# Kernel tuning notes

Measured on AMD Instinct MI355X. Metric: run time of the kernel, lower is better.

The kernel has to match this reference:

```python
import jax, jax.numpy as jnp
import numpy as np

BN_EPS = 1e-5
N_NODES = 100000
N_EDGES = 1600000
D = 128


def setup_inputs() -> dict:
    key = jax.random.key(0)
    ks = jax.random.split(key, 8)
    h = jax.random.normal(ks[0], (N_NODES, D), dtype=jnp.float32)
    snorm_n = jax.random.uniform(ks[1], (N_NODES, 1), dtype=jnp.float32)
    eps = jnp.zeros((1,), dtype=jnp.float32)
    W1 = jax.random.normal(ks[2], (D, D), dtype=jnp.float32) * (1.0 / np.sqrt(D))
    b1 = jnp.zeros((D,), dtype=jnp.float32)
    W2 = jax.random.normal(ks[3], (D, D), dtype=jnp.float32) * (1.0 / np.sqrt(D))
    b2 = jnp.zeros((D,), dtype=jnp.float32)
    bn_gamma = jnp.ones((D,), dtype=jnp.float32)
    bn_beta = jnp.zeros((D,), dtype=jnp.float32)
    src = jax.random.randint(ks[4], (N_EDGES,), 0, N_NODES, dtype=jnp.int32)
    dst = jax.random.randint(ks[5], (N_EDGES,), 0, N_NODES, dtype=jnp.int32)
    return {"h": h, "snorm_n": snorm_n, "eps": eps, "W1": W1, "b1": b1,
            "W2": W2, "b2": b2, "bn_gamma": bn_gamma, "bn_beta": bn_beta,
            "src": src, "dst": dst}


def reference(h, snorm_n, eps, W1, b1, W2, b2, bn_gamma, bn_beta, src, dst):
    h_in = h
    # message passing: copy_u + sum reduce -> scatter-add of h[src] into dst
    neigh = jax.ops.segment_sum(h[src], dst, num_segments=N_NODES)  # [N, D]
    x = (1.0 + eps[0]) * h + neigh
    # apply_func: 2-layer MLP (Linear -> ReLU -> Linear)
    x = jax.nn.relu(x @ W1 + b1) @ W2 + b2
    # graph norm w.r.t. graph sizes
    x = x * snorm_n
    # batch norm (training-mode batch statistics over nodes)
    mean = jnp.mean(x, axis=0)
    var = jnp.var(x, axis=0)
    x = (x - mean) * jax.lax.rsqrt(var + BN_EPS) * bn_gamma + bn_beta
    x = jax.nn.relu(x)
    # residual (in_dim == out_dim)
    x = h_in + x
    # dropout p=0.0 -> identity
    return x
```

## Files before the change

### kernel.cpp

```cpp
#include <hip/hip_runtime.h>

#define D 128
#define NN 100000
#define NE 1600000
#define SCAN_NBLK 98
#define GT_ROWS 128
#define GEMM_NT ((NN + GT_ROWS - 1) / GT_ROWS)
#define GEMM_GRID 256

__global__ __launch_bounds__(256) void count_kernel(
    const int* __restrict__ dst, int* __restrict__ cnt)
{
    int g4 = blockIdx.x * 256 + threadIdx.x;
    if (g4 >= NE / 4) return;
    int4 d = ((const int4*)dst)[g4];
    atomicAdd(&cnt[d.x], 1);
    atomicAdd(&cnt[d.y], 1);
    atomicAdd(&cnt[d.z], 1);
    atomicAdd(&cnt[d.w], 1);
}

__global__ __launch_bounds__(256) void scan_local_kernel(
    const int* __restrict__ cnt, int* __restrict__ pre, int* __restrict__ blkSum)
{
    __shared__ int lds[256];
    const int t = threadIdx.x;
    const int base = blockIdx.x * 1024 + t * 4;
    int4 v = {0, 0, 0, 0};
    if (base + 3 < NN) v = *(const int4*)&cnt[base];
    else {
        if (base + 0 < NN) v.x = cnt[base + 0];
        if (base + 1 < NN) v.y = cnt[base + 1];
        if (base + 2 < NN) v.z = cnt[base + 2];
        if (base + 3 < NN) v.w = cnt[base + 3];
    }
    const int s = v.x + v.y + v.z + v.w;
    lds[t] = s;
    __syncthreads();
    for (int off = 1; off < 256; off <<= 1) {
        int val = 0;
        if (t >= off) val = lds[t - off];
        __syncthreads();
        if (t >= off) lds[t] += val;
        __syncthreads();
    }
    const int excl = lds[t] - s;
    if (t == 255) blkSum[blockIdx.x] = lds[255];
    int4 o;
    o.x = excl;
    o.y = excl + v.x;
    o.z = excl + v.x + v.y;
    o.w = excl + v.x + v.y + v.z;
    if (base + 3 < NN) *(int4*)&pre[base] = o;
    else {
        if (base + 0 < NN) pre[base + 0] = o.x;
        if (base + 1 < NN) pre[base + 1] = o.y;
        if (base + 2 < NN) pre[base + 2] = o.z;
        if (base + 3 < NN) pre[base + 3] = o.w;
    }
}

__global__ __launch_bounds__(128) void scan_blk_kernel(
    const int* __restrict__ blkSum, int* __restrict__ blkOfs)
{
    __shared__ int lds[128];
    const int t = threadIdx.x;
    int s = (t < SCAN_NBLK) ? blkSum[t] : 0;
    lds[t] = s;
    __syncthreads();
    for (int off = 1; off < 128; off <<= 1) {
        int val = 0;
        if (t >= off) val = lds[t - off];
        __syncthreads();
        if (t >= off) lds[t] += val;
        __syncthreads();
    }
    blkOfs[t] = lds[t] - s;
}

__global__ __launch_bounds__(256) void scan_finish_kernel(
    const int* __restrict__ pre, const int* __restrict__ blkOfs,
    int* __restrict__ row_start, int* __restrict__ cursor)
{
    int n = blockIdx.x * 256 + threadIdx.x;
    if (n > NN) return;
    int v = (n == NN) ? NE : pre[n] + blkOfs[n >> 10];
    row_start[n] = v;
    if (n < NN) cursor[n] = v;
}

__global__ __launch_bounds__(256) void fill_kernel(
    const int* __restrict__ src, const int* __restrict__ dst,
    int* __restrict__ cursor, int* __restrict__ eidx)
{
    int e = blockIdx.x * 256 + threadIdx.x;
    if (e >= NE) return;
    int pos = atomicAdd(&cursor[dst[e]], 1);
    eidx[pos] = src[e];
}

__global__ __launch_bounds__(256) void gather_kernel(
    const float* __restrict__ h, const int* __restrict__ row_start,
    const int* __restrict__ eidx, const float* __restrict__ epsp,
    float* __restrict__ x)
{
    int gid  = blockIdx.x * 256 + threadIdx.x;
    int node = gid >> 5;
    int lane = gid & 31;
    if (node >= NN) return;
    const int s0 = row_start[node];
    const int s1 = row_start[node + 1];
    const float sc = 1.0f + epsp[0];
    float4 hv = ((const float4*)(h + (size_t)node * D))[lane];
    float ax = sc * hv.x, ay = sc * hv.y, az = sc * hv.z, aw = sc * hv.w;
    float bx = 0.f, by = 0.f, bz = 0.f, bw = 0.f;
    int e = s0;
    for (; e + 1 < s1; e += 2) {
        int sa = eidx[e];
        int sb = eidx[e + 1];
        float4 va = ((const float4*)(h + (size_t)sa * D))[lane];
        float4 vb = ((const float4*)(h + (size_t)sb * D))[lane];
        ax += va.x; ay += va.y; az += va.z; aw += va.w;
        bx += vb.x; by += vb.y; bz += vb.z; bw += vb.w;
    }
    if (e < s1) {
        int sa = eidx[e];
        float4 va = ((const float4*)(h + (size_t)sa * D))[lane];
        ax += va.x; ay += va.y; az += va.z; aw += va.w;
    }
    float4 o = {ax + bx, ay + by, az + bz, aw + bw};
    ((float4*)(x + (size_t)node * D))[lane] = o;
}

template <int MODE>
__global__ __launch_bounds__(256, 1) void gemm_kernel(
    const float* __restrict__ xin, const float* __restrict__ W,
    const float* __restrict__ bias, const float* __restrict__ snorm,
    float* __restrict__ out, double* __restrict__ stats)
{
    __shared__ float wl[D * D];
    __shared__ float xb[D * GT_ROWS];
    const int tid = threadIdx.x;

    {
        const float4* Wv = (const float4*)W;
        float4* wv = (float4*)wl;
#pragma unroll
        for (int i = 0; i < 16; ++i) wv[tid + i * 256] = Wv[tid + i * 256];
    }

    const int cg = tid & 15;
    const int rg = tid >> 4;
    const int ca = cg * 4;
    const int cb = 64 + cg * 4;

    float4 bva = ((const float4*)bias)[cg];
    float4 bvb = ((const float4*)bias)[16 + cg];

    float ssum[8], ssq[8];
#pragma unroll
    for (int j = 0; j < 8; ++j) { ssum[j] = 0.f; ssq[j] = 0.f; }

    float4 rstg[8];
    auto LOADH = [&](int t, int hk) {
        const int row0 = t * GT_ROWS;
#pragma unroll
        for (int i = 0; i < 8; ++i) {
            int idx = tid + i * 256;
            int row = idx >> 4;
            int kc  = (idx & 15) + hk * 16;
            int grow = row0 + row;
            rstg[i] = (grow < NN)
                ? ((const float4*)(xin + (size_t)grow * D))[kc]
                : make_float4(0.f, 0.f, 0.f, 0.f);
        }
    };
    auto WRITEH = [&](int hk) {
#pragma unroll
        for (int i = 0; i < 8; ++i) {
            int idx = tid + i * 256;
            int row = idx >> 4;
            int kc  = (idx & 15) + hk * 16;
            int c4  = (row >> 2) ^ (kc & 7);
            float v[4] = {rstg[i].x, rstg[i].y, rstg[i].z, rstg[i].w};
#pragma unroll
            for (int j = 0; j < 4; ++j)
                xb[(kc * 4 + j) * GT_ROWS + c4 * 4 + (row & 3)] = v[j];
        }
    };

    for (int t = blockIdx.x; t < GEMM_NT; t += GEMM_GRID) {
        float acc[8][8];
#pragma unroll
        for (int i = 0; i < 8; ++i)
#pragma unroll
            for (int j = 0; j < 8; ++j) acc[i][j] = 0.f;

        if (t == (int)blockIdx.x) LOADH(t, 0);
        __syncthreads();
        WRITEH(0);
        LOADH(t, 1);
        __syncthreads();

#pragma unroll 1
        for (int half = 0; half < 2; ++half) {
            const int k0 = half * 64;
#pragma unroll 4
            for (int kk = 0; kk < 64; ++kk) {
                const int k  = k0 + kk;
                const int sk = (k >> 2) & 7;
                float4 xa = *(const float4*)&xb[k * GT_ROWS + (((2 * rg) ^ sk) << 2)];
                float4 xc = *(const float4*)&xb[k * GT_ROWS + (((2 * rg + 1) ^ sk) << 2)];
                float4 wa = *(const float4*)&wl[k * D + ca];
                float4 wb = *(const float4*)&wl[k * D + cb];
                float xr[8] = {xa.x, xa.y, xa.z, xa.w, xc.x, xc.y, xc.z, xc.w};
                float wr[8] = {wa.x, wa.y, wa.z, wa.w, wb.x, wb.y, wb.z, wb.w};
#pragma unroll
                for (int i = 0; i < 8; ++i)
#pragma unroll
                    for (int j = 0; j < 8; ++j)
                        acc[i][j] = fmaf(xr[i], wr[j], acc[i][j]);
            }
            if (half == 0) {
                WRITEH(1);
                int tn = t + GEMM_GRID;
                if (tn < GEMM_NT) LOADH(tn, 0);
                __syncthreads();
            }
        }

#pragma unroll
        for (int i = 0; i < 8; ++i) {
            int row = t * GT_ROWS + rg * 8 + i;
            if (row < NN) {
                float oa[4], ob[4];
                if (MODE == 1) {
                    oa[0] = fmaxf(acc[i][0] + bva.x, 0.f);
                    oa[1] = fmaxf(acc[i][1] + bva.y, 0.f);
                    oa[2] = fmaxf(acc[i][2] + bva.z, 0.f);
                    oa[3] = fmaxf(acc[i][3] + bva.w, 0.f);
                    ob[0] = fmaxf(acc[i][4] + bvb.x, 0.f);
                    ob[1] = fmaxf(acc[i][5] + bvb.y, 0.f);
                    ob[2] = fmaxf(acc[i][6] + bvb.z, 0.f);
                    ob[3] = fmaxf(acc[i][7] + bvb.w, 0.f);
                } else {
                    const float sn = snorm[row];
                    oa[0] = (acc[i][0] + bva.x) * sn;
                    oa[1] = (acc[i][1] + bva.y) * sn;
                    oa[2] = (acc[i][2] + bva.z) * sn;
                    oa[3] = (acc[i][3] + bva.w) * sn;
                    ob[0] = (acc[i][4] + bvb.x) * sn;
                    ob[1] = (acc[i][5] + bvb.y) * sn;
                    ob[2] = (acc[i][6] + bvb.z) * sn;
                    ob[3] = (acc[i][7] + bvb.w) * sn;
#pragma unroll
                    for (int j = 0; j < 4; ++j) {
                        ssum[j]     += oa[j];  ssq[j]     += oa[j] * oa[j];
                        ssum[4 + j] += ob[j];  ssq[4 + j] += ob[j] * ob[j];
                    }
                }
                float* op = out + (size_t)row * D;
                *(float4*)&op[ca] = *(float4*)&oa[0];
                *(float4*)&op[cb] = *(float4*)&ob[0];
            }
        }
    }

    if (MODE == 2) {
        float* red = xb;
        __syncthreads();
#pragma unroll
        for (int j = 0; j < 4; ++j) {
            red[rg * D + ca + j] = ssum[j];
            red[rg * D + cb + j] = ssum[4 + j];
        }
        __syncthreads();
        if (tid < D) {
            float s = 0.f;
#pragma unroll
            for (int r = 0; r < 16; ++r) s += red[r * D + tid];
            atomicAdd(&stats[tid], (double)s);
        }
        __syncthreads();
#pragma unroll
        for (int j = 0; j < 4; ++j) {
            red[rg * D + ca + j] = ssq[j];
            red[rg * D + cb + j] = ssq[4 + j];
        }
        __syncthreads();
        if (tid < D) {
            float s = 0.f;
#pragma unroll
            for (int r = 0; r < 16; ++r) s += red[r * D + tid];
            atomicAdd(&stats[D + tid], (double)s);
        }
    }
}

__global__ void bn_prep_kernel(const double* __restrict__ stats,
                               const float* __restrict__ gamma,
                               const float* __restrict__ beta,
                               float* __restrict__ sc_sh)
{
    int c = threadIdx.x;
    double mean = stats[c] * (1.0 / NN);
    double var  = stats[D + c] * (1.0 / NN) - mean * mean;
    float rs = rsqrtf((float)var + 1e-5f);
    float sc = gamma[c] * rs;
    sc_sh[c]     = sc;
    sc_sh[D + c] = beta[c] - (float)mean * sc;
}

__global__ __launch_bounds__(256) void finalize_kernel(
    const float* __restrict__ y, const float* __restrict__ h,
    const float* __restrict__ sc_sh, float* __restrict__ out)
{
    int i  = blockIdx.x * 256 + threadIdx.x;
    int cf = i & 31;
    float4 yv = ((const float4*)y)[i];
    float4 hv = ((const float4*)h)[i];
    float4 sc = ((const float4*)sc_sh)[cf];
    float4 sh = ((const float4*)(sc_sh + D))[cf];
    float4 o;
    o.x = hv.x + fmaxf(fmaf(yv.x, sc.x, sh.x), 0.0f);
    o.y = hv.y + fmaxf(fmaf(yv.y, sc.y, sh.y), 0.0f);
    o.z = hv.z + fmaxf(fmaf(yv.z, sc.z, sh.z), 0.0f);
    o.w = hv.w + fmaxf(fmaf(yv.w, sc.w, sh.w), 0.0f);
    ((float4*)out)[i] = o;
}

extern "C" void kernel_launch(void* const* d_in, const int* in_sizes, int n_in,
                              void* d_out, int out_size, void* d_ws, size_t ws_size,
                              hipStream_t stream)
{
    const float* h     = (const float*)d_in[0];
    const float* snorm = (const float*)d_in[1];
    const float* eps   = (const float*)d_in[2];
    const float* W1    = (const float*)d_in[3];
    const float* b1    = (const float*)d_in[4];
    const float* W2    = (const float*)d_in[5];
    const float* b2    = (const float*)d_in[6];
    const float* gamma = (const float*)d_in[7];
    const float* beta  = (const float*)d_in[8];
    const int*   src   = (const int*)d_in[9];
    const int*   dst   = (const int*)d_in[10];
    float* out = (float*)d_out;

    char* ws = (char*)d_ws;
    const size_t BUF_BYTES = (size_t)NN * D * sizeof(float);
    float*  buf       = (float*)ws;
    double* stats     = (double*)(ws + BUF_BYTES);
    float*  sc_sh     = (float*)(ws + BUF_BYTES + 2048);
    char*   p         = ws + BUF_BYTES + 4096;
    int*    cnt       = (int*)p;            p += (size_t)NN * 4;
    int*    pre       = (int*)p;            p += (size_t)NN * 4;
    int*    row_start = (int*)p;            p += (size_t)(NN + 4) * 4;
    int*    cursor    = (int*)p;            p += (size_t)NN * 4;
    int*    blkSum    = (int*)p;            p += 512;
    int*    blkOfs    = (int*)p;            p += 512;
    int*    eidx      = (int*)p;

    hipMemsetAsync(cnt, 0, (size_t)NN * 4, stream);
    hipMemsetAsync(stats, 0, 2048, stream);

    count_kernel<<<(NE / 4 + 255) / 256, 256, 0, stream>>>(dst, cnt);
    scan_local_kernel<<<SCAN_NBLK, 256, 0, stream>>>(cnt, pre, blkSum);
    scan_blk_kernel<<<1, 128, 0, stream>>>(blkSum, blkOfs);
    scan_finish_kernel<<<(NN + 256) / 256 + 1, 256, 0, stream>>>(pre, blkOfs, row_start, cursor);
    fill_kernel<<<(NE + 255) / 256, 256, 0, stream>>>(src, dst, cursor, eidx);

    gather_kernel<<<NN * 32 / 256, 256, 0, stream>>>(h, row_start, eidx, eps, buf);

    gemm_kernel<1><<<GEMM_GRID, 256, 0, stream>>>(buf, W1, b1, nullptr, buf, nullptr);
    gemm_kernel<2><<<GEMM_GRID, 256, 0, stream>>>(buf, W2, b2, snorm, buf, stats);

    bn_prep_kernel<<<1, D, 0, stream>>>(stats, gamma, beta, sc_sh);
    finalize_kernel<<<NN * D / 4 / 256, 256, 0, stream>>>(buf, h, sc_sh, out);
}
```

Baseline: 566.2 us.

## Bin edges by destination range before CSR fill; read GEMM weights from global

Edges are pre-binned into 8 destination ranges, packed with their source index, during the counting pass. The fill kernel then processes each range separately so cursor atomics and eidx writes stay in a smaller address window. The GEMM drops the LDS copy of W and reads weights straight from global/cache, loads a whole 128-row tile per iteration, and raises occupancy to 2 blocks per CU with a 512-block grid. This trades an extra pass over src/dst and a staging buffer for better fill locality, and trades LDS weight reuse for higher occupancy.

Measured after the change: 577.9 us. +2.1%, slower.

```diff
diff --git a/kernel.cpp b/kernel.cpp
--- a/kernel.cpp
+++ b/kernel.cpp
@@ -6,18 +6,69 @@
 #define SCAN_NBLK 98
 #define GT_ROWS 128
 #define GEMM_NT ((NN + GT_ROWS - 1) / GT_ROWS)
-#define GEMM_GRID 256
-
-__global__ __launch_bounds__(256) void count_kernel(
-    const int* __restrict__ dst, int* __restrict__ cnt)
-{
-    int g4 = blockIdx.x * 256 + threadIdx.x;
-    if (g4 >= NE / 4) return;
-    int4 d = ((const int4*)dst)[g4];
-    atomicAdd(&cnt[d.x], 1);
-    atomicAdd(&cnt[d.y], 1);
-    atomicAdd(&cnt[d.z], 1);
-    atomicAdd(&cnt[d.w], 1);
+#define GEMM_GRID 512
+#define NRANGE 8
+#define RANGE_SZ 12500
+#define STREAM_CAP 204800
+#define BINA_GRID 256
+#define FILLB_GRID 1024
+
+__global__ void init8_kernel(unsigned int* __restrict__ gcur8)
+{
+    if (threadIdx.x < NRANGE) gcur8[threadIdx.x] = threadIdx.x * STREAM_CAP;
+}
+
+__global__ __launch_bounds__(256) void bin_count_kernel(
+    const int* __restrict__ src, const int* __restrict__ dst,
+    int* __restrict__ cnt, unsigned int* __restrict__ gcur8,
+    unsigned int* __restrict__ stream)
+{
+    __shared__ unsigned int cnt8[NRANGE], base8[NRANGE], off8[NRANGE];
+    const int tid = threadIdx.x;
+    if (tid < NRANGE) cnt8[tid] = 0;
+    __syncthreads();
+    const int NT4 = NE / 4;
+    for (int i4 = blockIdx.x * 256 + tid; i4 < NT4; i4 += BINA_GRID * 256) {
+        int4 d = ((const int4*)dst)[i4];
+        atomicAdd(&cnt[d.x], 1);
+        atomicAdd(&cnt[d.y], 1);
+        atomicAdd(&cnt[d.z], 1);
+        atomicAdd(&cnt[d.w], 1);
+        atomicAdd(&cnt8[d.x / RANGE_SZ], 1u);
+        atomicAdd(&cnt8[d.y / RANGE_SZ], 1u);
+        atomicAdd(&cnt8[d.z / RANGE_SZ], 1u);
+        atomicAdd(&cnt8[d.w / RANGE_SZ], 1u);
+    }
+    __syncthreads();
+    if (tid < NRANGE) {
+        base8[tid] = atomicAdd(&gcur8[tid], cnt8[tid]);
+        off8[tid]  = 0;
+    }
+    __syncthreads();
+    for (int i4 = blockIdx.x * 256 + tid; i4 < NT4; i4 += BINA_GRID * 256) {
+        int4 d = ((const int4*)dst)[i4];
+        int4 s = ((const int4*)src)[i4];
+        {
+            int r = d.x / RANGE_SZ; unsigned dl = (unsigned)(d.x - r * RANGE_SZ);
+            unsigned pos = base8[r] + atomicAdd(&off8[r], 1u);
+            stream[pos] = (dl << 17) | (unsigned)s.x;
+        }
+        {
+            int r = d.y / RANGE_SZ; unsigned dl = (unsigned)(d.y - r * RANGE_SZ);
+            unsigned pos = base8[r] + atomicAdd(&off8[r], 1u);
+            stream[pos] = (dl << 17) | (unsigned)s.y;
+        }
+        {
+            int r = d.z / RANGE_SZ; unsigned dl = (unsigned)(d.z - r * RANGE_SZ);
+            unsigned pos = base8[r] + atomicAdd(&off8[r], 1u);
+            stream[pos] = (dl << 17) | (unsigned)s.z;
+        }
+        {
+            int r = d.w / RANGE_SZ; unsigned dl = (unsigned)(d.w - r * RANGE_SZ);
+            unsigned pos = base8[r] + atomicAdd(&off8[r], 1u);
+            stream[pos] = (dl << 17) | (unsigned)s.w;
+        }
+    }
 }
 
 __global__ __launch_bounds__(256) void scan_local_kernel(
@@ -90,13 +141,21 @@
 }
 
 __global__ __launch_bounds__(256) void fill_kernel(
-    const int* __restrict__ src, const int* __restrict__ dst,
+    const unsigned int* __restrict__ stream, const unsigned int* __restrict__ gcur8,
     int* __restrict__ cursor, int* __restrict__ eidx)
 {
-    int e = blockIdx.x * 256 + threadIdx.x;
-    if (e >= NE) return;
-    int pos = atomicAdd(&cursor[dst[e]], 1);
-    eidx[pos] = src[e];
+    const int r = blockIdx.x & 7;
+    const int chunk = blockIdx.x >> 3;
+    const unsigned s1 = gcur8[r];
+    const unsigned stride = (FILLB_GRID / 8) * 256;
+    for (unsigned i = (unsigned)r * STREAM_CAP + chunk * 256 + threadIdx.x;
+         i < s1; i += stride) {
+        unsigned p = stream[i];
+        int s  = (int)(p & 0x1FFFFu);
+        int dn = r * RANGE_SZ + (int)(p >> 17);
+        int pos = atomicAdd(&cursor[dn], 1);
+        eidx[pos] = s;
+    }
 }
 
 __global__ __launch_bounds__(256) void gather_kernel(
@@ -133,26 +192,18 @@
 }
 
 template <int MODE>
-__global__ __launch_bounds__(256, 1) void gemm_kernel(
+__global__ __launch_bounds__(256, 2) void gemm_kernel(
     const float* __restrict__ xin, const float* __restrict__ W,
     const float* __restrict__ bias, const float* __restrict__ snorm,
     float* __restrict__ out, double* __restrict__ stats)
 {
-    __shared__ float wl[D * D];
     __shared__ float xb[D * GT_ROWS];
     const int tid = threadIdx.x;
-
-    {
-        const float4* Wv = (const float4*)W;
-        float4* wv = (float4*)wl;
-#pragma unroll
-        for (int i = 0; i < 16; ++i) wv[tid + i * 256] = Wv[tid + i * 256];
-    }
-
     const int cg = tid & 15;
     const int rg = tid >> 4;
     const int ca = cg * 4;
     const int cb = 64 + cg * 4;
+    const float4* Wv = (const float4*)W;
 
     float4 bva = ((const float4*)bias)[cg];
     float4 bvb = ((const float4*)bias)[16 + cg];
@@ -161,26 +212,26 @@
 #pragma unroll
     for (int j = 0; j < 8; ++j) { ssum[j] = 0.f; ssq[j] = 0.f; }
 
-    float4 rstg[8];
-    auto LOADH = [&](int t, int hk) {
+    float4 rstg[16];
+    auto LOADT = [&](int t) {
         const int row0 = t * GT_ROWS;
 #pragma unroll
-        for (int i = 0; i < 8; ++i) {
+        for (int i = 0; i < 16; ++i) {
             int idx = tid + i * 256;
-            int row = idx >> 4;
-            int kc  = (idx & 15) + hk * 16;
+            int row = idx >> 5;
+            int kc  = idx & 31;
             int grow = row0 + row;
             rstg[i] = (grow < NN)
                 ? ((const float4*)(xin + (size_t)grow * D))[kc]
                 : make_float4(0.f, 0.f, 0.f, 0.f);
         }
     };
-    auto WRITEH = [&](int hk) {
-#pragma unroll
-        for (int i = 0; i < 8; ++i) {
+    auto WRITET = [&]() {
+#pragma unroll
+        for (int i = 0; i < 16; ++i) {
             int idx = tid + i * 256;
-            int row = idx >> 4;
-            int kc  = (idx & 15) + hk * 16;
+            int row = idx >> 5;
+            int kc  = idx & 31;
             int c4  = (row >> 2) ^ (kc & 7);
             float v[4] = {rstg[i].x, rstg[i].y, rstg[i].z, rstg[i].w};
 #pragma unroll
@@ -189,45 +240,37 @@
         }
     };
 
+    bool first = true;
     for (int t = blockIdx.x; t < GEMM_NT; t += GEMM_GRID) {
+        if (first) { LOADT(t); first = false; }
+        __syncthreads();
+        WRITET();
+        __syncthreads();
+
         float acc[8][8];
 #pragma unroll
         for (int i = 0; i < 8; ++i)
 #pragma unroll
             for (int j = 0; j < 8; ++j) acc[i][j] = 0.f;
 
-        if (t == (int)blockIdx.x) LOADH(t, 0);
-        __syncthreads();
-        WRITEH(0);
-        LOADH(t, 1);
-        __syncthreads();
-
-#pragma unroll 1
-        for (int half = 0; half < 2; ++half) {
-            const int k0 = half * 64;
 #pragma unroll 4
-            for (int kk = 0; kk < 64; ++kk) {
-                const int k  = k0 + kk;
-                const int sk = (k >> 2) & 7;
-                float4 xa = *(const float4*)&xb[k * GT_ROWS + (((2 * rg) ^ sk) << 2)];
-                float4 xc = *(const float4*)&xb[k * GT_ROWS + (((2 * rg + 1) ^ sk) << 2)];
-                float4 wa = *(const float4*)&wl[k * D + ca];
-                float4 wb = *(const float4*)&wl[k * D + cb];
-                float xr[8] = {xa.x, xa.y, xa.z, xa.w, xc.x, xc.y, xc.z, xc.w};
-                float wr[8] = {wa.x, wa.y, wa.z, wa.w, wb.x, wb.y, wb.z, wb.w};
-#pragma unroll
-                for (int i = 0; i < 8; ++i)
-#pragma unroll
-                    for (int j = 0; j < 8; ++j)
-                        acc[i][j] = fmaf(xr[i], wr[j], acc[i][j]);
-            }
-            if (half == 0) {
-                WRITEH(1);
-                int tn = t + GEMM_GRID;
-                if (tn < GEMM_NT) LOADH(tn, 0);
-                __syncthreads();
-            }
-        }
+        for (int k = 0; k < D; ++k) {
+            const int sk = (k >> 2) & 7;
+            float4 xa = *(const float4*)&xb[k * GT_ROWS + (((rg * 2) ^ sk) << 2)];
+            float4 xc = *(const float4*)&xb[k * GT_ROWS + (((rg * 2 + 1) ^ sk) << 2)];
+            float4 wa = Wv[k * 32 + cg];
+            float4 wb = Wv[k * 32 + 16 + cg];
+            float xr[8] = {xa.x, xa.y, xa.z, xa.w, xc.x, xc.y, xc.z, xc.w};
+            float wr[8] = {wa.x, wa.y, wa.z, wa.w, wb.x, wb.y, wb.z, wb.w};
+#pragma unroll
+            for (int i = 0; i < 8; ++i)
+#pragma unroll
+                for (int j = 0; j < 8; ++j)
+                    acc[i][j] = fmaf(xr[i], wr[j], acc[i][j]);
+        }
+
+        int tn = t + GEMM_GRID;
+        if (tn < GEMM_NT) LOADT(tn);
 
 #pragma unroll
         for (int i = 0; i < 8; ++i) {
@@ -358,16 +401,19 @@
     int*    cursor    = (int*)p;            p += (size_t)NN * 4;
     int*    blkSum    = (int*)p;            p += 512;
     int*    blkOfs    = (int*)p;            p += 512;
-    int*    eidx      = (int*)p;
+    unsigned int* gcur8  = (unsigned int*)p;  p += 256;
+    int*    eidx      = (int*)p;            p += (size_t)NE * 4;
+    unsigned int* stream8 = (unsigned int*)p;
 
     hipMemsetAsync(cnt, 0, (size_t)NN * 4, stream);
     hipMemsetAsync(stats, 0, 2048, stream);
-
-    count_kernel<<<(NE / 4 + 255) / 256, 256, 0, stream>>>(dst, cnt);
+    init8_kernel<<<1, 64, 0, stream>>>(gcur8);
+
+    bin_count_kernel<<<BINA_GRID, 256, 0, stream>>>(src, dst, cnt, gcur8, stream8);
     scan_local_kernel<<<SCAN_NBLK, 256, 0, stream>>>(cnt, pre, blkSum);
     scan_blk_kernel<<<1, 128, 0, stream>>>(blkSum, blkOfs);
     scan_finish_kernel<<<(NN + 256) / 256 + 1, 256, 0, stream>>>(pre, blkOfs, row_start, cursor);
-    fill_kernel<<<(NE + 255) / 256, 256, 0, stream>>>(src, dst, cursor, eidx);
+    fill_kernel<<<FILLB_GRID, 256, 0, stream>>>(stream8, gcur8, cursor, eidx);
 
     gather_kernel<<<NN * 32 / 256, 256, 0, stream>>>(h, row_start, eidx, eps, buf);
 
```
